# Kernel optimization log

Measured on AMD Instinct MI355X. Metric: run time of the kernel, lower is better.

The kernel has to match this reference:

```python
import jax, jax.numpy as jnp
import numpy as np

T, D, H, FF, L = 4096, 512, 8, 2048, 6  # tokens, model dim, heads, ffn hidden, shared layers
HW = D // H  # head width = 64
N_SEG = 8
EPS = 1e-12


def setup_inputs() -> dict:
    key = jax.random.key(0)
    ks = jax.random.split(key, 16)
    s = 0.02

    def w(k, shape):
        return (jax.random.normal(k, shape, jnp.float32) * s)

    return {
        "h": jax.random.normal(ks[0], (T, D), jnp.float32),
        "seg_ids": jnp.sort(jax.random.randint(ks[1], (T,), 0, N_SEG, jnp.int32)),
        # attention projections (shared across layers, as in the torch module)
        "Wq": w(ks[2], (D, D)), "bq": jnp.zeros((D,), jnp.float32),
        "Wk": w(ks[3], (D, D)), "bk": jnp.zeros((D,), jnp.float32),
        "Wv": w(ks[4], (D, D)), "bv": jnp.zeros((D,), jnp.float32),
        "Wc": w(ks[5], (D, D)), "bc": jnp.zeros((D,), jnp.float32),
        # output projection
        "Wp": w(ks[6], (D, D)), "bp": jnp.zeros((D,), jnp.float32),
        # layer norms
        "g1": jnp.ones((D,), jnp.float32), "b1": jnp.zeros((D,), jnp.float32),
        "g2": jnp.ones((D,), jnp.float32), "b2": jnp.zeros((D,), jnp.float32),
        # position-wise FFN
        "W1": w(ks[7], (D, FF)), "fb1": jnp.zeros((FF,), jnp.float32),
        "W2": w(ks[8], (FF, D)), "fb2": jnp.zeros((D,), jnp.float32),
    }


def _layernorm(x, gamma, beta):
    # TF-style LN: eps inside the sqrt, biased variance
    u = x.mean(-1, keepdims=True)
    s = ((x - u) ** 2).mean(-1, keepdims=True)
    return gamma * (x - u) / jnp.sqrt(s + EPS) + beta


def _swish(x):
    return x * jax.nn.sigmoid(x)


def reference(h, seg_ids, Wq, bq, Wk, bk, Wv, bv, Wc, bc, Wp, bp,
              g1, b1, g2, b2, W1, fb1, W2, fb2):
    # Segment-local attention: equivalent to the torch per-split loop, since
    # softmax over a block-diagonal mask == per-segment softmax.
    mask = seg_ids[:, None] == seg_ids[None, :]  # [T, T]
    scale = 1.0 / np.sqrt(HW).astype(np.float32)
    for _ in range(L):  # shared weights across layers, as in the module
        prev = h
        q = (h @ Wq + bq).reshape(T, H, HW)
        k = (h @ Wk + bk).reshape(T, H, HW)
        v = (h @ Wv + bv).reshape(T, H, HW)
        c = h @ Wc + bc
        scores = jnp.einsum("thw,shw->hts", q, k) * scale  # [H, T, T]
        scores = jnp.where(mask[None], scores, jnp.float32(-1e30))
        att = jax.nn.softmax(scores, axis=-1)
        attn_out = jnp.einsum("hts,shw->thw", att, v).reshape(T, D) + c
        h = _layernorm(prev + attn_out @ Wp + bp, g1, b1)
        h = _layernorm(h + _swish(h @ W1 + fb1) @ W2 + fb2, g2, b2)
    return h
```

## Files before the change

kernel.cpp:

```cpp
#include <hip/hip_runtime.h>
#include <stdint.h>

#define TTOK 4096
#define DMODEL 512
#define NHEAD 8
#define FFDIM 2048
#define NLAYER 6

typedef short bf16x8 __attribute__((ext_vector_type(8)));
typedef float f32x4 __attribute__((ext_vector_type(4)));
typedef int v2i __attribute__((ext_vector_type(2)));

__device__ __forceinline__ unsigned short f2bf(float f) {
  union { float f; unsigned int u; } v; v.f = f;
  unsigned int u = v.u;
  unsigned int r = (u + 0x7FFFu + ((u >> 16) & 1u)) >> 16;
  return (unsigned short)r;
}

__device__ __forceinline__ float bf2f(unsigned short h) {
  union { unsigned int u; float f; } v; v.u = ((unsigned int)h) << 16;
  return v.f;
}

#define GLOAD_LDS16(gp, lp)                                                      \
  __builtin_amdgcn_global_load_lds(                                              \
      (const __attribute__((address_space(1))) unsigned int*)(gp),               \
      (__attribute__((address_space(3))) unsigned int*)(lp), 16, 0, 0)

__global__ void transpose_cast(const float* __restrict__ src, unsigned short* __restrict__ dst,
                               int K, int N) {
  __shared__ float tile[32][33];
  const int n0 = blockIdx.x * 32, k0 = blockIdx.y * 32;
  const int x = threadIdx.x, y = threadIdx.y;
#pragma unroll
  for (int yy = 0; yy < 32; yy += 8)
    tile[y + yy][x] = src[(size_t)(k0 + y + yy) * N + n0 + x];
  __syncthreads();
#pragma unroll
  for (int yy = 0; yy < 32; yy += 8)
    dst[(size_t)(n0 + yy + y) * K + k0 + x] = f2bf(tile[x][y + yy]);
}

__global__ void pack_bias(const float* __restrict__ bq, const float* __restrict__ bk,
                          const float* __restrict__ bv, const float* __restrict__ bc,
                          float* __restrict__ out) {
  int i = blockIdx.x * 256 + threadIdx.x;
  const float* src = (i < 512) ? bq : (i < 1024) ? bk : (i < 1536) ? bv : bc;
  out[i] = src[i & 511];
}

__global__ void cast_bf16(const float* __restrict__ src, unsigned short* __restrict__ dst, int n4) {
  int i = blockIdx.x * 256 + threadIdx.x;
  if (i < n4) {
    float4 v = ((const float4*)src)[i];
    uint2 o;
    o.x = (unsigned int)f2bf(v.x) | ((unsigned int)f2bf(v.y) << 16);
    o.y = (unsigned int)f2bf(v.z) | ((unsigned int)f2bf(v.w) << 16);
    ((uint2*)dst)[i] = o;
  }
}

__global__ void seg_bounds(const int* __restrict__ seg, int* __restrict__ ss,
                           int* __restrict__ se, int T) {
  const int t = blockIdx.x * 256 + threadIdx.x;
  if (t >= T) return;
  const int sid = seg[t];
  int lo = 0, hi = T;
  while (lo < hi) { int mid = (lo + hi) >> 1; if (seg[mid] < sid) lo = mid + 1; else hi = mid; }
  ss[t] = lo;
  lo = t; hi = T;
  while (lo < hi) { int mid = (lo + hi) >> 1; if (seg[mid] <= sid) lo = mid + 1; else hi = mid; }
  se[t] = lo;
}

template <int MODE, int MF, int WM>
__launch_bounds__(256)
__global__ void gemm_bf16(const unsigned short* __restrict__ A,
                          const unsigned short* __restrict__ Bt,
                          int M, int N, int K,
                          const float* __restrict__ bias,
                          const float* __restrict__ res,
                          float* __restrict__ outF,
                          unsigned short* __restrict__ outB) {
  constexpr int WN = 4 / WM;
  constexpr int BM = MF * 16 * WM;
  constexpr int BN = 64 * WN;
  __shared__ uint4 As[2][BM * 8];
  __shared__ uint4 Bs[2][BN * 8];
  const int tid = threadIdx.x;
  const int lane = tid & 63;
  const int wv = tid >> 6;
  const int wm = wv / WN, wn = wv % WN;
  const int l15 = lane & 15, l4 = lane >> 4;
  const int bm0 = blockIdx.x * BM;
  const int bn0 = blockIdx.y * BN;

  f32x4 acc[MF][4];
#pragma unroll
  for (int m = 0; m < MF; ++m)
#pragma unroll
    for (int n = 0; n < 4; ++n) acc[m][n] = (f32x4){0.f, 0.f, 0.f, 0.f};

  auto stage = [&](int b, int k0) {
#pragma unroll
    for (int i = 0; i < (BM * 8) / 256; ++i) {
      const int u = tid + i * 256;
      const int r = u >> 3;
      const int c = (u & 7) ^ (r & 7);
      GLOAD_LDS16(A + (size_t)(bm0 + r) * K + k0 + c * 8, &As[b][i * 256 + wv * 64]);
    }
#pragma unroll
    for (int i = 0; i < (BN * 8) / 256; ++i) {
      const int u = tid + i * 256;
      const int r = u >> 3;
      const int c = (u & 7) ^ (r & 7);
      GLOAD_LDS16(Bt + (size_t)(bn0 + r) * K + k0 + c * 8, &Bs[b][i * 256 + wv * 64]);
    }
  };

  const int nt = K >> 6;
  stage(0, 0);
  __syncthreads();
  int bufi = 0;
  for (int t = 0; t < nt; ++t) {
    if (t + 1 < nt) stage(bufi ^ 1, (t + 1) << 6);
#pragma unroll
    for (int kk = 0; kk < 2; ++kk) {
      bf16x8 af[MF], bfr[4];
#pragma unroll
      for (int m = 0; m < MF; ++m) {
        const int row = wm * (MF * 16) + m * 16 + l15;
        const int c = kk * 4 + l4;
        af[m] = *(const bf16x8*)&As[bufi][row * 8 + (c ^ (row & 7))];
      }
#pragma unroll
      for (int n = 0; n < 4; ++n) {
        const int row = wn * 64 + n * 16 + l15;
        const int c = kk * 4 + l4;
        bfr[n] = *(const bf16x8*)&Bs[bufi][row * 8 + (c ^ (row & 7))];
      }
#pragma unroll
      for (int m = 0; m < MF; ++m)
#pragma unroll
        for (int n = 0; n < 4; ++n)
          acc[m][n] = __builtin_amdgcn_mfma_f32_16x16x32_bf16(af[m], bfr[n], acc[m][n], 0, 0, 0);
    }
    __syncthreads();
    bufi ^= 1;
  }

  float bvals[4];
#pragma unroll
  for (int n = 0; n < 4; ++n) bvals[n] = bias[bn0 + wn * 64 + n * 16 + l15];

#pragma unroll
  for (int m = 0; m < MF; ++m) {
#pragma unroll
    for (int r = 0; r < 4; ++r) {
      const int R = bm0 + wm * (MF * 16) + m * 16 + l4 * 4 + r;
#pragma unroll
      for (int n = 0; n < 4; ++n) {
        const int C = bn0 + wn * 64 + n * 16 + l15;
        float v = acc[m][n][r] + bvals[n];
        if (MODE == 1) {
          v += res[(size_t)R * N + C];
          outF[(size_t)R * N + C] = v;
        } else if (MODE == 2) {
          v = v / (1.f + __expf(-v));
          outB[(size_t)R * N + C] = f2bf(v);
        } else {
          outB[(size_t)R * N + C] = f2bf(v);
        }
      }
    }
  }
}

__launch_bounds__(64)
__global__ void attn_mfma(const unsigned short* __restrict__ qkvcb,
                          const int* __restrict__ sstart,
                          const int* __restrict__ send,
                          unsigned short* __restrict__ aob) {
  __shared__ unsigned short Vt[4096];
  __shared__ unsigned short Pl[16 * 68];
  const int lane = threadIdx.x;
  const int l15 = lane & 15;
  const int g = lane >> 4;
  const int head = blockIdx.x & 7;
  const int q0 = (blockIdx.x >> 3) * 16;

  const size_t qbase = (size_t)(q0 + l15) * 2048 + head * 64;
  const bf16x8 qf0 = *(const bf16x8*)(qkvcb + qbase + g * 8);
  const bf16x8 qf1 = *(const bf16x8*)(qkvcb + qbase + 32 + g * 8);

  int sr[4], er[4];
#pragma unroll
  for (int r = 0; r < 4; ++r) {
    const int q = q0 + 4 * g + r;
    sr[r] = sstart[q];
    er[r] = send[q];
  }
  const int s0 = sstart[q0];
  const int e1 = send[q0 + 15];

  const int vtokrel = lane >> 1;
  const unsigned short* vsrc = qkvcb + 1024 + head * 64 + (lane & 1) * 8;

  bf16x8 kfa[4], kfb[4];
  auto LOADK = [&](int k0) {
#pragma unroll
    for (int n = 0; n < 4; ++n) {
      const size_t kb =
          (size_t)min(k0 + 16 * n + l15, TTOK - 1) * 2048 + 512 + head * 64;
      kfa[n] = *(const bf16x8*)(qkvcb + kb + g * 8);
      kfb[n] = *(const bf16x8*)(qkvcb + kb + 32 + g * 8);
    }
  };
  auto STAGEV = [&](int k0) {
#pragma unroll
    for (int i = 0; i < 8; ++i) {
      const int tok = min(k0 + vtokrel + (i & 1) * 32, TTOK - 1);
      GLOAD_LDS16(vsrc + (size_t)tok * 2048 + (i >> 1) * 16, Vt + i * 512);
    }
  };

  STAGEV(s0);
  LOADK(s0);

  float m_[4], l_[4];
  f32x4 o[4];
#pragma unroll
  for (int r = 0; r < 4; ++r) { m_[r] = -1e30f; l_[r] = 0.f; }
#pragma unroll
  for (int n = 0; n < 4; ++n) o[n] = (f32x4){0.f, 0.f, 0.f, 0.f};

  for (int k0 = s0; k0 < e1; k0 += 64) {
    f32x4 sac[4];
#pragma unroll
    for (int n = 0; n < 4; ++n) {
      f32x4 z = (f32x4){0.f, 0.f, 0.f, 0.f};
      z = __builtin_amdgcn_mfma_f32_16x16x32_bf16(qf0, kfa[n], z, 0, 0, 0);
      sac[n] = __builtin_amdgcn_mfma_f32_16x16x32_bf16(qf1, kfb[n], z, 0, 0, 0);
    }

    float pv[4][4];
    float pmax[4] = {-1e30f, -1e30f, -1e30f, -1e30f};
#pragma unroll
    for (int n = 0; n < 4; ++n) {
      const int col = k0 + 16 * n + l15;
#pragma unroll
      for (int r = 0; r < 4; ++r) {
        float v = sac[n][r] * 0.125f;
        if (col < sr[r] || col >= er[r]) v = -1e30f;
        pv[n][r] = v;
        pmax[r] = fmaxf(pmax[r], v);
      }
    }
    bool need = false;
#pragma unroll
    for (int r = 0; r < 4; ++r) need |= (pmax[r] > m_[r] + 8.f);
    if (__any(need)) {
      float tm[4];
#pragma unroll
      for (int r = 0; r < 4; ++r) tm[r] = pmax[r];
#pragma unroll
      for (int off = 1; off < 16; off <<= 1) {
#pragma unroll
        for (int r = 0; r < 4; ++r) tm[r] = fmaxf(tm[r], __shfl_xor(tm[r], off));
      }
      f32x4 corrv;
#pragma unroll
      for (int r = 0; r < 4; ++r) {
        const float nm = fmaxf(m_[r], tm[r]);
        const float corr = __expf(m_[r] - nm);
        m_[r] = nm;
        l_[r] *= corr;
        corrv[r] = corr;
      }
#pragma unroll
      for (int n = 0; n < 4; ++n) o[n] *= corrv;
    }
    float psum[4] = {0.f, 0.f, 0.f, 0.f};
#pragma unroll
    for (int n = 0; n < 4; ++n) {
#pragma unroll
      for (int r = 0; r < 4; ++r) {
        const float p = __expf(pv[n][r] - m_[r]);
        pv[n][r] = p;
        psum[r] += p;
      }
    }
#pragma unroll
    for (int off = 1; off < 16; off <<= 1) {
#pragma unroll
      for (int r = 0; r < 4; ++r) psum[r] += __shfl_xor(psum[r], off);
    }
#pragma unroll
    for (int r = 0; r < 4; ++r) l_[r] += psum[r];

#pragma unroll
    for (int n = 0; n < 4; ++n)
#pragma unroll
      for (int r = 0; r < 4; ++r)
        Pl[(4 * g + r) * 68 + 16 * n + l15] = f2bf(pv[n][r]);
    const bf16x8 pa0 = *(const bf16x8*)(Pl + l15 * 68 + g * 8);
    const bf16x8 pa1 = *(const bf16x8*)(Pl + l15 * 68 + 32 + g * 8);

    v2i t[16];
    {
      const __attribute__((address_space(3))) unsigned short* vb3 =
          ((const __attribute__((address_space(3))) unsigned short*)Vt) +
          g * 128 + l15 * 4;
      asm volatile("ds_read_b64_tr_b16 %0, %1"              : "=v"(t[0])  : "v"(vb3));
      asm volatile("ds_read_b64_tr_b16 %0, %1 offset:128"   : "=v"(t[1])  : "v"(vb3));
      asm volatile("ds_read_b64_tr_b16 %0, %1 offset:1024"  : "=v"(t[2])  : "v"(vb3));
      asm volatile("ds_read_b64_tr_b16 %0, %1 offset:1152"  : "=v"(t[3])  : "v"(vb3));
      asm volatile("ds_read_b64_tr_b16 %0, %1 offset:2048"  : "=v"(t[4])  : "v"(vb3));
      asm volatile("ds_read_b64_tr_b16 %0, %1 offset:2176"  : "=v"(t[5])  : "v"(vb3));
      asm volatile("ds_read_b64_tr_b16 %0, %1 offset:3072"  : "=v"(t[6])  : "v"(vb3));
      asm volatile("ds_read_b64_tr_b16 %0, %1 offset:3200"  : "=v"(t[7])  : "v"(vb3));
      asm volatile("ds_read_b64_tr_b16 %0, %1 offset:4096"  : "=v"(t[8])  : "v"(vb3));
      asm volatile("ds_read_b64_tr_b16 %0, %1 offset:4224"  : "=v"(t[9])  : "v"(vb3));
      asm volatile("ds_read_b64_tr_b16 %0, %1 offset:5120"  : "=v"(t[10]) : "v"(vb3));
      asm volatile("ds_read_b64_tr_b16 %0, %1 offset:5248"  : "=v"(t[11]) : "v"(vb3));
      asm volatile("ds_read_b64_tr_b16 %0, %1 offset:6144"  : "=v"(t[12]) : "v"(vb3));
      asm volatile("ds_read_b64_tr_b16 %0, %1 offset:6272"  : "=v"(t[13]) : "v"(vb3));
      asm volatile("ds_read_b64_tr_b16 %0, %1 offset:7168"  : "=v"(t[14]) : "v"(vb3));
      asm volatile("ds_read_b64_tr_b16 %0, %1 offset:7296"  : "=v"(t[15]) : "v"(vb3));
      asm volatile("s_waitcnt lgkmcnt(0)" ::: "memory");
      __builtin_amdgcn_sched_barrier(0);
    }

    const int k0n = (k0 + 64 < e1) ? (k0 + 64) : s0;
    STAGEV(k0n);
    LOADK(k0n);

    union VU { v2i p[2]; bf16x8 f; };
#pragma unroll
    for (int n = 0; n < 4; ++n) {
      VU u0, u1;
      u0.p[0] = t[4 * n];     u0.p[1] = t[4 * n + 1];
      u1.p[0] = t[4 * n + 2]; u1.p[1] = t[4 * n + 3];
      o[n] = __builtin_amdgcn_mfma_f32_16x16x32_bf16(pa0, u0.f, o[n], 0, 0, 0);
      o[n] = __builtin_amdgcn_mfma_f32_16x16x32_bf16(pa1, u1.f, o[n], 0, 0, 0);
    }
  }

  float rl[4];
#pragma unroll
  for (int r = 0; r < 4; ++r) rl[r] = 1.f / l_[r];
#pragma unroll
  for (int n = 0; n < 4; ++n) {
#pragma unroll
    for (int r = 0; r < 4; ++r) {
      const int q = q0 + 4 * g + r;
      const int d = head * 64 + 16 * n + l15;
      const float cv = bf2f(qkvcb[(size_t)q * 2048 + 1536 + d]);
      aob[(size_t)q * 512 + d] = f2bf(o[n][r] * rl[r] + cv);
    }
  }
}

__launch_bounds__(64)
__global__ void ln_kernel(const float* __restrict__ x, const float* __restrict__ g,
                          const float* __restrict__ b, float* __restrict__ outF,
                          unsigned short* __restrict__ outB) {
  const int row = blockIdx.x;
  const int lane = threadIdx.x;
  const float4* xr = (const float4*)(x + (size_t)row * 512);
  float4 a = xr[lane * 2], c = xr[lane * 2 + 1];
  float s = a.x + a.y + a.z + a.w + c.x + c.y + c.z + c.w;
  float sq = a.x * a.x + a.y * a.y + a.z * a.z + a.w * a.w +
             c.x * c.x + c.y * c.y + c.z * c.z + c.w * c.w;
#pragma unroll
  for (int off = 1; off < 64; off <<= 1) {
    s += __shfl_xor(s, off);
    sq += __shfl_xor(sq, off);
  }
  const float mean = s * (1.f / 512.f);
  const float var = sq * (1.f / 512.f) - mean * mean;
  const float rstd = rsqrtf(var + 1e-12f);
  const float4* gr = (const float4*)g;
  const float4* br = (const float4*)b;
  float4 g0 = gr[lane * 2], g1v = gr[lane * 2 + 1];
  float4 b0 = br[lane * 2], b1v = br[lane * 2 + 1];
  float4 y0, y1;
  y0.x = (a.x - mean) * rstd * g0.x + b0.x;
  y0.y = (a.y - mean) * rstd * g0.y + b0.y;
  y0.z = (a.z - mean) * rstd * g0.z + b0.z;
  y0.w = (a.w - mean) * rstd * g0.w + b0.w;
  y1.x = (c.x - mean) * rstd * g1v.x + b1v.x;
  y1.y = (c.y - mean) * rstd * g1v.y + b1v.y;
  y1.z = (c.z - mean) * rstd * g1v.z + b1v.z;
  y1.w = (c.w - mean) * rstd * g1v.w + b1v.w;
  float4* of = (float4*)(outF + (size_t)row * 512);
  of[lane * 2] = y0;
  of[lane * 2 + 1] = y1;
  uint4 ob;
  ob.x = (unsigned int)f2bf(y0.x) | ((unsigned int)f2bf(y0.y) << 16);
  ob.y = (unsigned int)f2bf(y0.z) | ((unsigned int)f2bf(y0.w) << 16);
  ob.z = (unsigned int)f2bf(y1.x) | ((unsigned int)f2bf(y1.y) << 16);
  ob.w = (unsigned int)f2bf(y1.z) | ((unsigned int)f2bf(y1.w) << 16);
  ((uint4*)(outB + (size_t)row * 512))[lane] = ob;
}

extern "C" void kernel_launch(void* const* d_in, const int* in_sizes, int n_in,
                              void* d_out, int out_size, void* d_ws, size_t ws_size,
                              hipStream_t stream) {
  const float* h_in = (const float*)d_in[0];
  const int* seg = (const int*)d_in[1];
  const float* Wq = (const float*)d_in[2];
  const float* bq = (const float*)d_in[3];
  const float* Wk = (const float*)d_in[4];
  const float* bk = (const float*)d_in[5];
  const float* Wv = (const float*)d_in[6];
  const float* bv = (const float*)d_in[7];
  const float* Wc = (const float*)d_in[8];
  const float* bc = (const float*)d_in[9];
  const float* Wp = (const float*)d_in[10];
  const float* bp = (const float*)d_in[11];
  const float* g1 = (const float*)d_in[12];
  const float* b1 = (const float*)d_in[13];
  const float* g2 = (const float*)d_in[14];
  const float* b2 = (const float*)d_in[15];
  const float* W1 = (const float*)d_in[16];
  const float* fb1 = (const float*)d_in[17];
  const float* W2 = (const float*)d_in[18];
  const float* fb2 = (const float*)d_in[19];
  float* outp = (float*)d_out;

  char* p = (char*)d_ws;
  auto alloc = [&](size_t bytes) {
    char* r = p;
    p += (bytes + 255) & ~(size_t)255;
    return r;
  };
  unsigned short* wqkvcb = (unsigned short*)alloc((size_t)2048 * 512 * 2);
  unsigned short* wpb = (unsigned short*)alloc((size_t)512 * 512 * 2);
  unsigned short* w1b = (unsigned short*)alloc((size_t)2048 * 512 * 2);
  unsigned short* w2b = (unsigned short*)alloc((size_t)512 * 2048 * 2);
  float* bqkvc = (float*)alloc(2048 * 4);
  unsigned short* hb = (unsigned short*)alloc((size_t)TTOK * 512 * 2);
  unsigned short* qkvcb = (unsigned short*)alloc((size_t)TTOK * 2048 * 2);
  unsigned short* aob = (unsigned short*)alloc((size_t)TTOK * 512 * 2);
  float* xbuf = (float*)alloc((size_t)TTOK * 512 * 4);
  float* h1 = (float*)alloc((size_t)TTOK * 512 * 4);
  unsigned short* h1b = (unsigned short*)alloc((size_t)TTOK * 512 * 2);
  unsigned short* f1b = (unsigned short*)alloc((size_t)TTOK * 2048 * 2);
  float* hcur = (float*)alloc((size_t)TTOK * 512 * 4);
  int* sstart = (int*)alloc(TTOK * 4);
  int* send = (int*)alloc(TTOK * 4);

  dim3 tb(32, 8);
  transpose_cast<<<dim3(16, 16), tb, 0, stream>>>(Wq, wqkvcb + 0 * 512 * 512, 512, 512);
  transpose_cast<<<dim3(16, 16), tb, 0, stream>>>(Wk, wqkvcb + 1 * 512 * 512, 512, 512);
  transpose_cast<<<dim3(16, 16), tb, 0, stream>>>(Wv, wqkvcb + 2 * 512 * 512, 512, 512);
  transpose_cast<<<dim3(16, 16), tb, 0, stream>>>(Wc, wqkvcb + 3 * 512 * 512, 512, 512);
  transpose_cast<<<dim3(16, 16), tb, 0, stream>>>(Wp, wpb, 512, 512);
  transpose_cast<<<dim3(64, 16), tb, 0, stream>>>(W1, w1b, 512, 2048);
  transpose_cast<<<dim3(16, 64), tb, 0, stream>>>(W2, w2b, 2048, 512);
  pack_bias<<<8, 256, 0, stream>>>(bq, bk, bv, bc, bqkvc);
  cast_bf16<<<2048, 256, 0, stream>>>(h_in, hb, TTOK * 512 / 4);
  seg_bounds<<<16, 256, 0, stream>>>(seg, sstart, send, TTOK);

  const float* resp = h_in;
  for (int layer = 0; layer < NLAYER; ++layer) {
    gemm_bf16<0, 4, 2><<<dim3(32, 16), 256, 0, stream>>>(hb, wqkvcb, TTOK, 2048, 512,
                                                         bqkvc, nullptr, nullptr, qkvcb);
    attn_mfma<<<dim3(2048), 64, 0, stream>>>(qkvcb, sstart, send, aob);
    gemm_bf16<1, 1, 4><<<dim3(64, 8), 256, 0, stream>>>(aob, wpb, TTOK, 512, 512,
                                                        bp, resp, xbuf, nullptr);
    ln_kernel<<<TTOK, 64, 0, stream>>>(xbuf, g1, b1, h1, h1b);
    gemm_bf16<2, 4, 2><<<dim3(32, 16), 256, 0, stream>>>(h1b, w1b, TTOK, 2048, 512,
                                                         fb1, nullptr, nullptr, f1b);
    gemm_bf16<1, 1, 4><<<dim3(64, 8), 256, 0, stream>>>(f1b, w2b, TTOK, 512, 2048,
                                                        fb2, h1, xbuf, nullptr);
    float* lnout = (layer == NLAYER - 1) ? outp : hcur;
    ln_kernel<<<TTOK, 64, 0, stream>>>(xbuf, g2, b2, lnout, hb);
    resp = hcur;
  }
}
```

Before: 751.4 us.

## Fuse output projection GEMM with LayerNorm; compute softmax row sums via MFMA

Adds a gemm_ln kernel where each 512-thread block computes a full 16-row strip of the attention output projection, then applies bias, residual and LayerNorm in-register. This removes the separate ln_kernel launch and the fp32 round trip through xbuf. The fused GEMM reads operands straight from global memory without LDS staging and launches only 256 blocks, so its GEMM part may run slower. In attention, the softmax denominator now comes from an extra MFMA against a ones vector on the bf16-rounded probabilities instead of shuffle reductions, which changes the rounding of the normaliser slightly.

```diff
diff --git a/kernel.cpp b/kernel.cpp
--- a/kernel.cpp
+++ b/kernel.cpp
@@ -177,6 +177,95 @@
   }
 }
 
+__launch_bounds__(512)
+__global__ void gemm_ln(const unsigned short* __restrict__ A,
+                        const unsigned short* __restrict__ Bt,
+                        int K,
+                        const float* __restrict__ bias,
+                        const float* __restrict__ res,
+                        const float* __restrict__ gamma,
+                        const float* __restrict__ beta,
+                        float* __restrict__ outF,
+                        unsigned short* __restrict__ outB) {
+  __shared__ float red[8][16][2];
+  const int tid = threadIdx.x;
+  const int lane = tid & 63;
+  const int wn = tid >> 6;
+  const int l15 = lane & 15, l4 = lane >> 4;
+  const int bm0 = blockIdx.x * 16;
+
+  f32x4 acc[4];
+#pragma unroll
+  for (int n = 0; n < 4; ++n) acc[n] = (f32x4){0.f, 0.f, 0.f, 0.f};
+
+  for (int k0 = 0; k0 < K; k0 += 32) {
+    const bf16x8 af = *(const bf16x8*)(A + (size_t)(bm0 + l15) * K + k0 + l4 * 8);
+#pragma unroll
+    for (int n = 0; n < 4; ++n) {
+      const int col = wn * 64 + n * 16 + l15;
+      const bf16x8 bfr = *(const bf16x8*)(Bt + (size_t)col * K + k0 + l4 * 8);
+      acc[n] = __builtin_amdgcn_mfma_f32_16x16x32_bf16(af, bfr, acc[n], 0, 0, 0);
+    }
+  }
+
+  const int row_l = l4 * 4;
+  float vals[4][4];
+  float bsum[4] = {0.f, 0.f, 0.f, 0.f}, bsq[4] = {0.f, 0.f, 0.f, 0.f};
+#pragma unroll
+  for (int n = 0; n < 4; ++n) {
+    const int col = wn * 64 + n * 16 + l15;
+    const float bn = bias[col];
+#pragma unroll
+    for (int r = 0; r < 4; ++r) {
+      const float v = acc[n][r] + bn + res[(size_t)(bm0 + row_l + r) * 512 + col];
+      vals[n][r] = v;
+      bsum[r] += v;
+      bsq[r] += v * v;
+    }
+  }
+#pragma unroll
+  for (int off = 1; off < 16; off <<= 1) {
+#pragma unroll
+    for (int r = 0; r < 4; ++r) {
+      bsum[r] += __shfl_xor(bsum[r], off);
+      bsq[r] += __shfl_xor(bsq[r], off);
+    }
+  }
+  if (l15 == 0) {
+#pragma unroll
+    for (int r = 0; r < 4; ++r) {
+      red[wn][row_l + r][0] = bsum[r];
+      red[wn][row_l + r][1] = bsq[r];
+    }
+  }
+  __syncthreads();
+  float mean[4], rstd[4];
+#pragma unroll
+  for (int r = 0; r < 4; ++r) {
+    float S = 0.f, Q = 0.f;
+#pragma unroll
+    for (int w = 0; w < 8; ++w) {
+      S += red[w][row_l + r][0];
+      Q += red[w][row_l + r][1];
+    }
+    const float mu = S * (1.f / 512.f);
+    mean[r] = mu;
+    rstd[r] = rsqrtf(Q * (1.f / 512.f) - mu * mu + 1e-12f);
+  }
+#pragma unroll
+  for (int n = 0; n < 4; ++n) {
+    const int col = wn * 64 + n * 16 + l15;
+    const float gm = gamma[col], bt = beta[col];
+#pragma unroll
+    for (int r = 0; r < 4; ++r) {
+      const float y = (vals[n][r] - mean[r]) * rstd[r] * gm + bt;
+      const size_t idx = (size_t)(bm0 + row_l + r) * 512 + col;
+      outF[idx] = y;
+      outB[idx] = f2bf(y);
+    }
+  }
+}
+
 __launch_bounds__(64)
 __global__ void attn_mfma(const unsigned short* __restrict__ qkvcb,
                           const int* __restrict__ sstart,
@@ -193,6 +282,8 @@
   const size_t qbase = (size_t)(q0 + l15) * 2048 + head * 64;
   const bf16x8 qf0 = *(const bf16x8*)(qkvcb + qbase + g * 8);
   const bf16x8 qf1 = *(const bf16x8*)(qkvcb + qbase + 32 + g * 8);
+  const bf16x8 ones = {(short)0x3F80, (short)0x3F80, (short)0x3F80, (short)0x3F80,
+                       (short)0x3F80, (short)0x3F80, (short)0x3F80, (short)0x3F80};
 
   int sr[4], er[4];
 #pragma unroll
@@ -281,23 +372,10 @@
 #pragma unroll
       for (int n = 0; n < 4; ++n) o[n] *= corrv;
     }
-    float psum[4] = {0.f, 0.f, 0.f, 0.f};
-#pragma unroll
-    for (int n = 0; n < 4; ++n) {
-#pragma unroll
-      for (int r = 0; r < 4; ++r) {
-        const float p = __expf(pv[n][r] - m_[r]);
-        pv[n][r] = p;
-        psum[r] += p;
-      }
-    }
-#pragma unroll
-    for (int off = 1; off < 16; off <<= 1) {
-#pragma unroll
-      for (int r = 0; r < 4; ++r) psum[r] += __shfl_xor(psum[r], off);
-    }
-#pragma unroll
-    for (int r = 0; r < 4; ++r) l_[r] += psum[r];
+#pragma unroll
+    for (int n = 0; n < 4; ++n)
+#pragma unroll
+      for (int r = 0; r < 4; ++r) pv[n][r] = __expf(pv[n][r] - m_[r]);
 
 #pragma unroll
     for (int n = 0; n < 4; ++n)
@@ -344,6 +422,13 @@
       u1.p[0] = t[4 * n + 2]; u1.p[1] = t[4 * n + 3];
       o[n] = __builtin_amdgcn_mfma_f32_16x16x32_bf16(pa0, u0.f, o[n], 0, 0, 0);
       o[n] = __builtin_amdgcn_mfma_f32_16x16x32_bf16(pa1, u1.f, o[n], 0, 0, 0);
+    }
+    {
+      f32x4 lacc = (f32x4){0.f, 0.f, 0.f, 0.f};
+      lacc = __builtin_amdgcn_mfma_f32_16x16x32_bf16(pa0, ones, lacc, 0, 0, 0);
+      lacc = __builtin_amdgcn_mfma_f32_16x16x32_bf16(pa1, ones, lacc, 0, 0, 0);
+#pragma unroll
+      for (int r = 0; r < 4; ++r) l_[r] += lacc[r];
     }
   }
 
@@ -469,9 +554,7 @@
     gemm_bf16<0, 4, 2><<<dim3(32, 16), 256, 0, stream>>>(hb, wqkvcb, TTOK, 2048, 512,
                                                          bqkvc, nullptr, nullptr, qkvcb);
     attn_mfma<<<dim3(2048), 64, 0, stream>>>(qkvcb, sstart, send, aob);
-    gemm_bf16<1, 1, 4><<<dim3(64, 8), 256, 0, stream>>>(aob, wpb, TTOK, 512, 512,
-                                                        bp, resp, xbuf, nullptr);
-    ln_kernel<<<TTOK, 64, 0, stream>>>(xbuf, g1, b1, h1, h1b);
+    gemm_ln<<<dim3(256), 512, 0, stream>>>(aob, wpb, 512, bp, resp, g1, b1, h1, h1b);
     gemm_bf16<2, 4, 2><<<dim3(32, 16), 256, 0, stream>>>(h1b, w1b, TTOK, 2048, 512,
                                                          fb1, nullptr, nullptr, f1b);
     gemm_bf16<1, 1, 4><<<dim3(64, 8), 256, 0, stream>>>(f1b, w2b, TTOK, 512, 2048,
```

Measured after the change: 812.8 us. 1.08x slower.

## Widen attention KV tile to 128 and compute row sums via MFMA with ones

Applied to the files above, without the earlier changes.

The attention kernel now processes 128 keys per iteration instead of 64, double-sizing the V staging buffer in LDS and the P tile, and issuing twice as many K fragment loads and MFMAs per step. The softmax row-sum is no longer built with per-lane adds and 16-lane shuffles. Instead it is computed by multiplying the bf16 P tile with a vector of ones on the matrix cores, which also makes l use the same bf16-rounded probabilities as the PV product. The goal is to halve loop overhead and the number of max and rescale checks and to remove shuffle reductions. In exchange, register and LDS pressure rise, and short segments waste more masked work.

```diff
diff --git a/kernel.cpp b/kernel.cpp
--- a/kernel.cpp
+++ b/kernel.cpp
@@ -182,8 +182,8 @@
                           const int* __restrict__ sstart,
                           const int* __restrict__ send,
                           unsigned short* __restrict__ aob) {
-  __shared__ unsigned short Vt[4096];
-  __shared__ unsigned short Pl[16 * 68];
+  __shared__ unsigned short Vt[2][4096];
+  __shared__ unsigned short Pl[16 * 136];
   const int lane = threadIdx.x;
   const int l15 = lane & 15;
   const int g = lane >> 4;
@@ -193,6 +193,8 @@
   const size_t qbase = (size_t)(q0 + l15) * 2048 + head * 64;
   const bf16x8 qf0 = *(const bf16x8*)(qkvcb + qbase + g * 8);
   const bf16x8 qf1 = *(const bf16x8*)(qkvcb + qbase + 32 + g * 8);
+  const bf16x8 ones = {(short)0x3F80, (short)0x3F80, (short)0x3F80, (short)0x3F80,
+                       (short)0x3F80, (short)0x3F80, (short)0x3F80, (short)0x3F80};
 
   int sr[4], er[4];
 #pragma unroll
@@ -207,25 +209,26 @@
   const int vtokrel = lane >> 1;
   const unsigned short* vsrc = qkvcb + 1024 + head * 64 + (lane & 1) * 8;
 
-  bf16x8 kfa[4], kfb[4];
+  bf16x8 kfa[8], kfb[8];
   auto LOADK = [&](int k0) {
 #pragma unroll
-    for (int n = 0; n < 4; ++n) {
+    for (int n = 0; n < 8; ++n) {
       const size_t kb =
           (size_t)min(k0 + 16 * n + l15, TTOK - 1) * 2048 + 512 + head * 64;
       kfa[n] = *(const bf16x8*)(qkvcb + kb + g * 8);
       kfb[n] = *(const bf16x8*)(qkvcb + kb + 32 + g * 8);
     }
   };
-  auto STAGEV = [&](int k0) {
+  auto STAGEV = [&](int k0, int h) {
 #pragma unroll
     for (int i = 0; i < 8; ++i) {
       const int tok = min(k0 + vtokrel + (i & 1) * 32, TTOK - 1);
-      GLOAD_LDS16(vsrc + (size_t)tok * 2048 + (i >> 1) * 16, Vt + i * 512);
+      GLOAD_LDS16(vsrc + (size_t)tok * 2048 + (i >> 1) * 16, &Vt[h][i * 512]);
     }
   };
 
-  STAGEV(s0);
+  STAGEV(s0, 0);
+  STAGEV(s0 + 64, 1);
   LOADK(s0);
 
   float m_[4], l_[4];
@@ -235,19 +238,19 @@
 #pragma unroll
   for (int n = 0; n < 4; ++n) o[n] = (f32x4){0.f, 0.f, 0.f, 0.f};
 
-  for (int k0 = s0; k0 < e1; k0 += 64) {
-    f32x4 sac[4];
-#pragma unroll
-    for (int n = 0; n < 4; ++n) {
+  for (int k0 = s0; k0 < e1; k0 += 128) {
+    f32x4 sac[8];
+#pragma unroll
+    for (int n = 0; n < 8; ++n) {
       f32x4 z = (f32x4){0.f, 0.f, 0.f, 0.f};
       z = __builtin_amdgcn_mfma_f32_16x16x32_bf16(qf0, kfa[n], z, 0, 0, 0);
       sac[n] = __builtin_amdgcn_mfma_f32_16x16x32_bf16(qf1, kfb[n], z, 0, 0, 0);
     }
 
-    float pv[4][4];
+    float pv[8][4];
     float pmax[4] = {-1e30f, -1e30f, -1e30f, -1e30f};
 #pragma unroll
-    for (int n = 0; n < 4; ++n) {
+    for (int n = 0; n < 8; ++n) {
       const int col = k0 + 16 * n + l15;
 #pragma unroll
       for (int r = 0; r < 4; ++r) {
@@ -281,69 +284,88 @@
 #pragma unroll
       for (int n = 0; n < 4; ++n) o[n] *= corrv;
     }
-    float psum[4] = {0.f, 0.f, 0.f, 0.f};
-#pragma unroll
-    for (int n = 0; n < 4; ++n) {
-#pragma unroll
-      for (int r = 0; r < 4; ++r) {
-        const float p = __expf(pv[n][r] - m_[r]);
-        pv[n][r] = p;
-        psum[r] += p;
-      }
-    }
-#pragma unroll
-    for (int off = 1; off < 16; off <<= 1) {
-#pragma unroll
-      for (int r = 0; r < 4; ++r) psum[r] += __shfl_xor(psum[r], off);
-    }
-#pragma unroll
-    for (int r = 0; r < 4; ++r) l_[r] += psum[r];
-
-#pragma unroll
-    for (int n = 0; n < 4; ++n)
+#pragma unroll
+    for (int n = 0; n < 8; ++n)
+#pragma unroll
+      for (int r = 0; r < 4; ++r) pv[n][r] = __expf(pv[n][r] - m_[r]);
+
+#pragma unroll
+    for (int n = 0; n < 8; ++n)
 #pragma unroll
       for (int r = 0; r < 4; ++r)
-        Pl[(4 * g + r) * 68 + 16 * n + l15] = f2bf(pv[n][r]);
-    const bf16x8 pa0 = *(const bf16x8*)(Pl + l15 * 68 + g * 8);
-    const bf16x8 pa1 = *(const bf16x8*)(Pl + l15 * 68 + 32 + g * 8);
-
-    v2i t[16];
+        Pl[(4 * g + r) * 136 + 16 * n + l15] = f2bf(pv[n][r]);
+    const bf16x8 pa0 = *(const bf16x8*)(Pl + l15 * 136 + g * 8);
+    const bf16x8 pa1 = *(const bf16x8*)(Pl + l15 * 136 + 32 + g * 8);
+    const bf16x8 pa2 = *(const bf16x8*)(Pl + l15 * 136 + 64 + g * 8);
+    const bf16x8 pa3 = *(const bf16x8*)(Pl + l15 * 136 + 96 + g * 8);
+
+    v2i t0[16], t1[16];
     {
       const __attribute__((address_space(3))) unsigned short* vb3 =
-          ((const __attribute__((address_space(3))) unsigned short*)Vt) +
+          ((const __attribute__((address_space(3))) unsigned short*)&Vt[0][0]) +
           g * 128 + l15 * 4;
-      asm volatile("ds_read_b64_tr_b16 %0, %1"              : "=v"(t[0])  : "v"(vb3));
-      asm volatile("ds_read_b64_tr_b16 %0, %1 offset:128"   : "=v"(t[1])  : "v"(vb3));
-      asm volatile("ds_read_b64_tr_b16 %0, %1 offset:1024"  : "=v"(t[2])  : "v"(vb3));
-      asm volatile("ds_read_b64_tr_b16 %0, %1 offset:1152"  : "=v"(t[3])  : "v"(vb3));
-      asm volatile("ds_read_b64_tr_b16 %0, %1 offset:2048"  : "=v"(t[4])  : "v"(vb3));
-      asm volatile("ds_read_b64_tr_b16 %0, %1 offset:2176"  : "=v"(t[5])  : "v"(vb3));
-      asm volatile("ds_read_b64_tr_b16 %0, %1 offset:3072"  : "=v"(t[6])  : "v"(vb3));
-      asm volatile("ds_read_b64_tr_b16 %0, %1 offset:3200"  : "=v"(t[7])  : "v"(vb3));
-      asm volatile("ds_read_b64_tr_b16 %0, %1 offset:4096"  : "=v"(t[8])  : "v"(vb3));
-      asm volatile("ds_read_b64_tr_b16 %0, %1 offset:4224"  : "=v"(t[9])  : "v"(vb3));
-      asm volatile("ds_read_b64_tr_b16 %0, %1 offset:5120"  : "=v"(t[10]) : "v"(vb3));
-      asm volatile("ds_read_b64_tr_b16 %0, %1 offset:5248"  : "=v"(t[11]) : "v"(vb3));
-      asm volatile("ds_read_b64_tr_b16 %0, %1 offset:6144"  : "=v"(t[12]) : "v"(vb3));
-      asm volatile("ds_read_b64_tr_b16 %0, %1 offset:6272"  : "=v"(t[13]) : "v"(vb3));
-      asm volatile("ds_read_b64_tr_b16 %0, %1 offset:7168"  : "=v"(t[14]) : "v"(vb3));
-      asm volatile("ds_read_b64_tr_b16 %0, %1 offset:7296"  : "=v"(t[15]) : "v"(vb3));
+      asm volatile("ds_read_b64_tr_b16 %0, %1"               : "=v"(t0[0])  : "v"(vb3));
+      asm volatile("ds_read_b64_tr_b16 %0, %1 offset:128"    : "=v"(t0[1])  : "v"(vb3));
+      asm volatile("ds_read_b64_tr_b16 %0, %1 offset:1024"   : "=v"(t0[2])  : "v"(vb3));
+      asm volatile("ds_read_b64_tr_b16 %0, %1 offset:1152"   : "=v"(t0[3])  : "v"(vb3));
+      asm volatile("ds_read_b64_tr_b16 %0, %1 offset:2048"   : "=v"(t0[4])  : "v"(vb3));
+      asm volatile("ds_read_b64_tr_b16 %0, %1 offset:2176"   : "=v"(t0[5])  : "v"(vb3));
+      asm volatile("ds_read_b64_tr_b16 %0, %1 offset:3072"   : "=v"(t0[6])  : "v"(vb3));
+      asm volatile("ds_read_b64_tr_b16 %0, %1 offset:3200"   : "=v"(t0[7])  : "v"(vb3));
+      asm volatile("ds_read_b64_tr_b16 %0, %1 offset:4096"   : "=v"(t0[8])  : "v"(vb3));
+      asm volatile("ds_read_b64_tr_b16 %0, %1 offset:4224"   : "=v"(t0[9])  : "v"(vb3));
+      asm volatile("ds_read_b64_tr_b16 %0, %1 offset:5120"   : "=v"(t0[10]) : "v"(vb3));
+      asm volatile("ds_read_b64_tr_b16 %0, %1 offset:5248"   : "=v"(t0[11]) : "v"(vb3));
+      asm volatile("ds_read_b64_tr_b16 %0, %1 offset:6144"   : "=v"(t0[12]) : "v"(vb3));
+      asm volatile("ds_read_b64_tr_b16 %0, %1 offset:6272"   : "=v"(t0[13]) : "v"(vb3));
+      asm volatile("ds_read_b64_tr_b16 %0, %1 offset:7168"   : "=v"(t0[14]) : "v"(vb3));
+      asm volatile("ds_read_b64_tr_b16 %0, %1 offset:7296"   : "=v"(t0[15]) : "v"(vb3));
+      asm volatile("ds_read_b64_tr_b16 %0, %1 offset:8192"   : "=v"(t1[0])  : "v"(vb3));
+      asm volatile("ds_read_b64_tr_b16 %0, %1 offset:8320"   : "=v"(t1[1])  : "v"(vb3));
+      asm volatile("ds_read_b64_tr_b16 %0, %1 offset:9216"   : "=v"(t1[2])  : "v"(vb3));
+      asm volatile("ds_read_b64_tr_b16 %0, %1 offset:9344"   : "=v"(t1[3])  : "v"(vb3));
+      asm volatile("ds_read_b64_tr_b16 %0, %1 offset:10240"  : "=v"(t1[4])  : "v"(vb3));
+      asm volatile("ds_read_b64_tr_b16 %0, %1 offset:10368"  : "=v"(t1[5])  : "v"(vb3));
+      asm volatile("ds_read_b64_tr_b16 %0, %1 offset:11264"  : "=v"(t1[6])  : "v"(vb3));
+      asm volatile("ds_read_b64_tr_b16 %0, %1 offset:11392"  : "=v"(t1[7])  : "v"(vb3));
+      asm volatile("ds_read_b64_tr_b16 %0, %1 offset:12288"  : "=v"(t1[8])  : "v"(vb3));
+      asm volatile("ds_read_b64_tr_b16 %0, %1 offset:12416"  : "=v"(t1[9])  : "v"(vb3));
+      asm volatile("ds_read_b64_tr_b16 %0, %1 offset:13312"  : "=v"(t1[10]) : "v"(vb3));
+      asm volatile("ds_read_b64_tr_b16 %0, %1 offset:13440"  : "=v"(t1[11]) : "v"(vb3));
+      asm volatile("ds_read_b64_tr_b16 %0, %1 offset:14336"  : "=v"(t1[12]) : "v"(vb3));
+      asm volatile("ds_read_b64_tr_b16 %0, %1 offset:14464"  : "=v"(t1[13]) : "v"(vb3));
+      asm volatile("ds_read_b64_tr_b16 %0, %1 offset:15360"  : "=v"(t1[14]) : "v"(vb3));
+      asm volatile("ds_read_b64_tr_b16 %0, %1 offset:15488"  : "=v"(t1[15]) : "v"(vb3));
       asm volatile("s_waitcnt lgkmcnt(0)" ::: "memory");
       __builtin_amdgcn_sched_barrier(0);
     }
 
-    const int k0n = (k0 + 64 < e1) ? (k0 + 64) : s0;
-    STAGEV(k0n);
+    const int k0n = (k0 + 128 < e1) ? (k0 + 128) : s0;
+    STAGEV(k0n, 0);
+    STAGEV(k0n + 64, 1);
     LOADK(k0n);
 
     union VU { v2i p[2]; bf16x8 f; };
 #pragma unroll
     for (int n = 0; n < 4; ++n) {
-      VU u0, u1;
-      u0.p[0] = t[4 * n];     u0.p[1] = t[4 * n + 1];
-      u1.p[0] = t[4 * n + 2]; u1.p[1] = t[4 * n + 3];
+      VU u0, u1, w0, w1;
+      u0.p[0] = t0[4 * n];     u0.p[1] = t0[4 * n + 1];
+      u1.p[0] = t0[4 * n + 2]; u1.p[1] = t0[4 * n + 3];
+      w0.p[0] = t1[4 * n];     w0.p[1] = t1[4 * n + 1];
+      w1.p[0] = t1[4 * n + 2]; w1.p[1] = t1[4 * n + 3];
       o[n] = __builtin_amdgcn_mfma_f32_16x16x32_bf16(pa0, u0.f, o[n], 0, 0, 0);
       o[n] = __builtin_amdgcn_mfma_f32_16x16x32_bf16(pa1, u1.f, o[n], 0, 0, 0);
+      o[n] = __builtin_amdgcn_mfma_f32_16x16x32_bf16(pa2, w0.f, o[n], 0, 0, 0);
+      o[n] = __builtin_amdgcn_mfma_f32_16x16x32_bf16(pa3, w1.f, o[n], 0, 0, 0);
+    }
+    {
+      f32x4 lacc = (f32x4){0.f, 0.f, 0.f, 0.f};
+      lacc = __builtin_amdgcn_mfma_f32_16x16x32_bf16(pa0, ones, lacc, 0, 0, 0);
+      lacc = __builtin_amdgcn_mfma_f32_16x16x32_bf16(pa1, ones, lacc, 0, 0, 0);
+      lacc = __builtin_amdgcn_mfma_f32_16x16x32_bf16(pa2, ones, lacc, 0, 0, 0);
+      lacc = __builtin_amdgcn_mfma_f32_16x16x32_bf16(pa3, ones, lacc, 0, 0, 0);
+#pragma unroll
+      for (int r = 0; r < 4; ++r) l_[r] += lacc[r];
     }
   }
 
```

Measured after the change: 750.0 us. Within noise of the previous version (-0.2%).
